# Optimization experiments

Measured on AMD Instinct MI355X. Metric: run time of the kernel, lower is better.

Reference implementation:

```python
import jax, jax.numpy as jnp
import numpy as np

H = 16      # n_heads
D = 1024    # d_model
DK = D // H # head dim


def setup_inputs() -> dict:
    key = jax.random.key(0)
    ks = jax.random.split(key, 11)
    B, S = 4, 2048
    std = 1.0 / np.sqrt(D)
    inp = {
        "query": jax.random.normal(ks[0], (B, S, D), jnp.float32),
        "key": jax.random.normal(ks[1], (B, S, D), jnp.float32),
        "value": jax.random.normal(ks[2], (B, S, D), jnp.float32),
        "Wq": jax.random.normal(ks[3], (D, D), jnp.float32) * std,
        "bq": jnp.zeros((D,), jnp.float32),
        "Wk": jax.random.normal(ks[4], (D, D), jnp.float32) * std,
        "bk": jnp.zeros((D,), jnp.float32),
        "Wv": jax.random.normal(ks[5], (D, D), jnp.float32) * std,
        "bv": jnp.zeros((D,), jnp.float32),
        "Wo": jax.random.normal(ks[6], (D, D), jnp.float32) * std,
        "bo": jnp.zeros((D,), jnp.float32),
    }
    return inp


def reference(query, key, value, Wq, bq, Wk, bk, Wv, bv, Wo, bo):
    B, S, _ = query.shape
    # QKV projections (nn.Linear), then split heads: [B, S, H, DK]
    q = (query @ Wq + bq).reshape(B, S, H, DK)
    k = (key @ Wk + bk).reshape(B, S, H, DK)
    v = (value @ Wv + bv).reshape(B, S, H, DK)
    # Memory-efficient attention computes exactly softmax(QK^T/sqrt(dk))V
    scale = 1.0 / np.sqrt(DK).astype(np.float32)
    scores = jnp.einsum("bqhd,bkhd->bhqk", q, k) * scale  # [B, H, S, S]
    attn = jax.nn.softmax(scores, axis=-1)
    x = jnp.einsum("bhqk,bkhd->bqhd", attn, v)            # [B, S, H, DK]
    x = x.reshape(B, S, H * DK)
    return x @ Wo + bo
```

## Files before the change

kernel.cpp:

```cpp
#include <hip/hip_runtime.h>
#include <hip/hip_bf16.h>

typedef short short8 __attribute__((ext_vector_type(8)));
typedef float f32x4 __attribute__((ext_vector_type(4)));
typedef float f32x16 __attribute__((ext_vector_type(16)));
typedef unsigned short u16;
typedef unsigned int u32;

#define HD 16
#define DMODEL 1024
#define DKH 64
#define SEQ 2048
#define QSCALE 0.18033688f

typedef const __attribute__((address_space(1))) void gvoid;
typedef __attribute__((address_space(3))) void lvoid;

__device__ inline u16 f2bf(float f) {
  unsigned int x = __builtin_bit_cast(unsigned int, f);
  unsigned int r = (x + 0x7fffu + ((x >> 16) & 1u)) >> 16;
  return (u16)r;
}

__device__ inline float fexp2(float x) {
#if __has_builtin(__builtin_amdgcn_exp2f)
  return __builtin_amdgcn_exp2f(x);
#else
  return __expf(x * 0.69314718f);
#endif
}

__device__ inline u32 cvtpk(float lo, float hi_) {
  u32 r;
  asm("v_cvt_pk_bf16_f32 %0, %1, %2" : "=v"(r) : "v"(lo), "v"(hi_));
  return r;
}

__device__ inline void pswap(u32& a, u32& b) {
  asm volatile("v_permlane32_swap_b32 %0, %1" : "+v"(a), "+v"(b));
}

__device__ inline f32x4 mfma16(short8 a, short8 b, f32x4 c) {
  return __builtin_amdgcn_mfma_f32_16x16x32_bf16(a, b, c, 0, 0, 0);
}
__device__ inline f32x16 mfma32(short8 a, short8 b, f32x16 c) {
  return __builtin_amdgcn_mfma_f32_32x32x16_bf16(a, b, c, 0, 0, 0);
}

__global__ __launch_bounds__(256) void prep_kernel(const float* __restrict__ q,
                                                   const float* __restrict__ k,
                                                   const float* __restrict__ v,
                                                   const float* __restrict__ W0,
                                                   const float* __restrict__ W1,
                                                   const float* __restrict__ W2,
                                                   const float* __restrict__ W3,
                                                   u16* __restrict__ Qf,
                                                   u16* __restrict__ Kf,
                                                   u16* __restrict__ Vf,
                                                   u16* __restrict__ WT) {
  const int z = blockIdx.z;
  if (z < 3) {
    const float* src = z == 0 ? q : z == 1 ? k : v;
    u16* dst = z == 0 ? Qf : z == 1 ? Kf : Vf;
    const int nthr = gridDim.x * 256;
    for (size_t i = blockIdx.x * 256 + threadIdx.x; i < (size_t)(SEQ * 4) * DMODEL / 8; i += nthr) {
      const float4 a0 = *(const float4*)(src + i * 8);
      const float4 a1 = *(const float4*)(src + i * 8 + 4);
      u32 tmp[4] = {cvtpk(a0.x, a0.y), cvtpk(a0.z, a0.w),
                    cvtpk(a1.x, a1.y), cvtpk(a1.z, a1.w)};
      *(uint4*)(dst + i * 8) = *(uint4*)tmp;
    }
  } else {
    __shared__ float tile[64][65];
    const int b = blockIdx.x;
    const int w = b >> 8;
    const int n0 = (b & 15) * 64, k0 = ((b >> 4) & 15) * 64;
    const float* W = w == 0 ? W0 : w == 1 ? W1 : w == 2 ? W2 : W3;
    u16* out = WT + (size_t)w * DMODEL * DMODEL;
    int tx = threadIdx.x & 63, ty = threadIdx.x >> 6;
    for (int i = 0; i < 16; i++) {
      int r = ty + i * 4;
      tile[r][tx] = W[(size_t)(k0 + r) * DMODEL + n0 + tx];
    }
    __syncthreads();
    for (int i = 0; i < 16; i++) {
      int r = ty + i * 4;
      out[(size_t)(n0 + r) * DMODEL + k0 + tx] = f2bf(tile[tx][r]);
    }
  }
}

__global__ __launch_bounds__(256, 2) void gemm_qkv(const u16* __restrict__ Qf,
                                                   const u16* __restrict__ Kf,
                                                   const u16* __restrict__ Vf,
                                                   const u16* __restrict__ WT,
                                                   const float* __restrict__ bq,
                                                   const float* __restrict__ bk,
                                                   const float* __restrict__ bv,
                                                   u16* __restrict__ Qb,
                                                   u16* __restrict__ Kb,
                                                   u16* __restrict__ Vtb) {
  __shared__ u16 As[2][128 * 64];
  __shared__ u16 Bs[2][128 * 64];
  const int b = blockIdx.x;
  const int xcd = b & 7, slot = b >> 3;
  const int nidx = slot & 7, pl = slot >> 3;
  const int pg = xcd * 24 + pl;
  const int z = pg >> 6, by = pg & 63;

  const u16* A = z == 0 ? Qf : z == 1 ? Kf : Vf;
  const u16* Bt = WT + (size_t)z * DMODEL * DMODEL;
  const float* bias = z == 0 ? bq : z == 1 ? bk : bv;
  u16* Cv = z == 0 ? Qb : z == 1 ? Kb : Vtb;
  const float scale = z == 0 ? QSCALE : 1.0f;
  const bool vtrans = (z == 2);

  const int m0 = by * 128, n0 = nidx * 128;
  const int tid = threadIdx.x;
  const int lane = tid & 63, wid = tid >> 6;
  const int g = lane >> 4, c = lane & 15;
  const int wr = (wid >> 1) * 64, wc = (wid & 1) * 64;

  const int trow = tid >> 3;
  const int tcolb = (tid & 7) << 4;
  const int swr = (c & 7) << 4;
  f32x4 acc[4][4] = {};

#define STAGE_AB(buf, kk0)                                                            \
  _Pragma("unroll") for (int p = 0; p < 4; ++p) {                                     \
    const int row = p * 32 + trow;                                                    \
    const int scol = tcolb ^ ((row & 7) << 4);                                        \
    __builtin_amdgcn_global_load_lds(                                                 \
        (gvoid*)((const char*)A + ((size_t)(m0 + row) * DMODEL + (kk0)) * 2 + scol),  \
        (lvoid*)((char*)&As[buf][0] + row * 128 + tcolb), 16, 0, 0);                  \
    __builtin_amdgcn_global_load_lds(                                                 \
        (gvoid*)((const char*)Bt + ((size_t)(n0 + row) * DMODEL + (kk0)) * 2 + scol), \
        (lvoid*)((char*)&Bs[buf][0] + row * 128 + tcolb), 16, 0, 0);                  \
  }

  STAGE_AB(0, 0);
  STAGE_AB(1, 64);
  __syncthreads();

  for (int t = 0; t < 16; ++t) {
    const int cur = t & 1;
    short8 af[4][2], bfr[4][2];
#pragma unroll
    for (int kk = 0; kk < 2; ++kk) {
#pragma unroll
      for (int mi = 0; mi < 4; ++mi)
        af[mi][kk] = *(const short8*)((const char*)&As[cur][0] + (wr + mi * 16 + c) * 128 + ((kk * 64 + g * 16) ^ swr));
#pragma unroll
      for (int ni = 0; ni < 4; ++ni)
        bfr[ni][kk] = *(const short8*)((const char*)&Bs[cur][0] + (wc + ni * 16 + c) * 128 + ((kk * 64 + g * 16) ^ swr));
    }
    __builtin_amdgcn_s_setprio(1);
#pragma unroll
    for (int kk = 0; kk < 2; ++kk)
#pragma unroll
      for (int mi = 0; mi < 4; ++mi)
#pragma unroll
        for (int ni = 0; ni < 4; ++ni)
          acc[mi][ni] = mfma16(af[mi][kk], bfr[ni][kk], acc[mi][ni]);
    __builtin_amdgcn_s_setprio(0);
    __syncthreads();
    if (t < 14) STAGE_AB(cur, (t + 2) * 64);
  }
#undef STAGE_AB

  for (int ni = 0; ni < 4; ++ni) {
    const int colg = n0 + wc + ni * 16 + c;
    const float bv_ = bias[colg];
    for (int mi = 0; mi < 4; ++mi) {
      const int rowb = m0 + wr + mi * 16 + g * 4;
      const int bb = rowb >> 11, s = rowb & 2047;
      const int h = colg >> 6, dk = colg & 63;
      if (!vtrans) {
        const size_t base = ((size_t)(bb * HD + h)) * SEQ;
        for (int j = 0; j < 4; ++j)
          Cv[(base + s + j) * DKH + dk] = f2bf((acc[mi][ni][j] + bv_) * scale);
      } else {
        const size_t base = ((size_t)(bb * HD + h) * DKH + dk) * SEQ + s;
        ushort4 u;
        u.x = f2bf(acc[mi][ni][0] + bv_);
        u.y = f2bf(acc[mi][ni][1] + bv_);
        u.z = f2bf(acc[mi][ni][2] + bv_);
        u.w = f2bf(acc[mi][ni][3] + bv_);
        *(ushort4*)(&Cv[base]) = u;
      }
    }
  }
}

__global__ __launch_bounds__(256, 2) void gemm_out(const u16* __restrict__ A,
                                                   const u16* __restrict__ Bt,
                                                   const float* __restrict__ bias,
                                                   float* __restrict__ C) {
  __shared__ u16 As[2][128 * 64];
  __shared__ u16 Bs[2][128 * 64];
  const int b = blockIdx.x;
  const int xcd = b & 7, slot = b >> 3;
  const int nidx = slot & 7, pl = slot >> 3;
  const int by = xcd * 8 + pl;

  const int m0 = by * 128, n0 = nidx * 128;
  const int tid = threadIdx.x;
  const int lane = tid & 63, wid = tid >> 6;
  const int g = lane >> 4, c = lane & 15;
  const int wr = (wid >> 1) * 64, wc = (wid & 1) * 64;

  const int trow = tid >> 3;
  const int tcolb = (tid & 7) << 4;
  const int swr = (c & 7) << 4;
  f32x4 acc[4][4] = {};

#define STAGE_AB(buf, kk0)                                                            \
  _Pragma("unroll") for (int p = 0; p < 4; ++p) {                                     \
    const int row = p * 32 + trow;                                                    \
    const int scol = tcolb ^ ((row & 7) << 4);                                        \
    __builtin_amdgcn_global_load_lds(                                                 \
        (gvoid*)((const char*)A + ((size_t)(m0 + row) * DMODEL + (kk0)) * 2 + scol),  \
        (lvoid*)((char*)&As[buf][0] + row * 128 + tcolb), 16, 0, 0);                  \
    __builtin_amdgcn_global_load_lds(                                                 \
        (gvoid*)((const char*)Bt + ((size_t)(n0 + row) * DMODEL + (kk0)) * 2 + scol), \
        (lvoid*)((char*)&Bs[buf][0] + row * 128 + tcolb), 16, 0, 0);                  \
  }

  STAGE_AB(0, 0);
  STAGE_AB(1, 64);
  __syncthreads();

  for (int t = 0; t < 16; ++t) {
    const int cur = t & 1;
    short8 af[4][2], bfr[4][2];
#pragma unroll
    for (int kk = 0; kk < 2; ++kk) {
#pragma unroll
      for (int mi = 0; mi < 4; ++mi)
        af[mi][kk] = *(const short8*)((const char*)&As[cur][0] + (wr + mi * 16 + c) * 128 + ((kk * 64 + g * 16) ^ swr));
#pragma unroll
      for (int ni = 0; ni < 4; ++ni)
        bfr[ni][kk] = *(const short8*)((const char*)&Bs[cur][0] + (wc + ni * 16 + c) * 128 + ((kk * 64 + g * 16) ^ swr));
    }
    __builtin_amdgcn_s_setprio(1);
#pragma unroll
    for (int kk = 0; kk < 2; ++kk)
#pragma unroll
      for (int mi = 0; mi < 4; ++mi)
#pragma unroll
        for (int ni = 0; ni < 4; ++ni)
          acc[mi][ni] = mfma16(af[mi][kk], bfr[ni][kk], acc[mi][ni]);
    __builtin_amdgcn_s_setprio(0);
    __syncthreads();
    if (t < 14) STAGE_AB(cur, (t + 2) * 64);
  }
#undef STAGE_AB

  for (int ni = 0; ni < 4; ++ni) {
    const int colg = n0 + wc + ni * 16 + c;
    const float bv = bias[colg];
    for (int mi = 0; mi < 4; ++mi) {
      const int rowb = m0 + wr + mi * 16 + g * 4;
      for (int j = 0; j < 4; ++j)
        C[(size_t)(rowb + j) * DMODEL + colg] = acc[mi][ni][j] + bv;
    }
  }
}

__global__ __launch_bounds__(256, 4) void attn_kernel(const u16* __restrict__ Q,
                                                      const u16* __restrict__ K,
                                                      const u16* __restrict__ Vt,
                                                      u16* __restrict__ X) {
  __shared__ char ldsmem[2][2][8192];
  const int tid = threadIdx.x;
  const int lane = tid & 63, wid = tid >> 6;
  const int c5 = lane & 31, hi = lane >> 5;

  const int blk = blockIdx.x;
  const int work = (blk & 7) * 128 + (blk >> 3);
  const int qt = work & 15, bh = work >> 4;

  const int q0 = qt * 128 + wid * 32;
  const u16* qb = Q + (size_t)bh * SEQ * DKH;
  const char* kbB = (const char*)(K + (size_t)bh * SEQ * DKH);
  const char* vbB = (const char*)(Vt + (size_t)bh * DKH * SEQ);

  short8 qf[4];
#pragma unroll
  for (int ks = 0; ks < 4; ++ks)
    qf[ks] = *(const short8*)(qb + (size_t)(q0 + c5) * DKH + ks * 16 + hi * 8);

  const int srow = tid >> 3;
  const int scolb = (tid & 7) << 4;
  const int scol = scolb ^ ((srow & 7) << 4);

  const int fswz = (c5 & 7) << 4;
  int cofs[4];
#pragma unroll
  for (int ks = 0; ks < 4; ++ks) cofs[ks] = ((ks * 32 + hi * 16) ^ fswz);

  f32x16 oacc[2] = {};
  float lrun = 0.f;

#pragma unroll
  for (int r32 = 0; r32 < 64; r32 += 32) {
    __builtin_amdgcn_global_load_lds(
        (gvoid*)(kbB + (size_t)(r32 + srow) * 128 + scol),
        (lvoid*)(&ldsmem[0][0][(r32 + srow) * 128 + scolb]), 16, 0, 0);
    __builtin_amdgcn_global_load_lds(
        (gvoid*)(vbB + (size_t)(r32 + srow) * (SEQ * 2) + scol),
        (lvoid*)(&ldsmem[0][1][(r32 + srow) * 128 + scolb]), 16, 0, 0);
  }
  __syncthreads();

#pragma unroll 2
  for (int t = 0; t < 32; ++t) {
    const int buf = t & 1;
    if (t < 31) {
      const size_t kv1 = (size_t)(t + 1) * 64;
#pragma unroll
      for (int r32 = 0; r32 < 64; r32 += 32) {
        __builtin_amdgcn_global_load_lds(
            (gvoid*)(kbB + (kv1 + r32 + srow) * 128 + scol),
            (lvoid*)(&ldsmem[buf ^ 1][0][(r32 + srow) * 128 + scolb]), 16, 0, 0);
        __builtin_amdgcn_global_load_lds(
            (gvoid*)(vbB + (size_t)(r32 + srow) * (SEQ * 2) + kv1 * 2 + scol),
            (lvoid*)(&ldsmem[buf ^ 1][1][(r32 + srow) * 128 + scolb]), 16, 0, 0);
      }
    }

    const char* bK = &ldsmem[buf][0][0];
    const char* bV = &ldsmem[buf][1][0];

    f32x16 sacc[2] = {};
#pragma unroll
    for (int kt = 0; kt < 2; ++kt) {
      short8 kf[4];
#pragma unroll
      for (int ks = 0; ks < 4; ++ks)
        kf[ks] = *(const short8*)(bK + (kt * 32 + c5) * 128 + cofs[ks]);
#pragma unroll
      for (int ks = 0; ks < 4; ++ks)
        sacc[kt] = mfma32(kf[ks], qf[ks], sacc[kt]);
    }

    float rs = 0.f;
    u32 W[2][8];
#pragma unroll
    for (int kt = 0; kt < 2; ++kt)
#pragma unroll
      for (int j = 0; j < 8; ++j) {
        float p0 = fexp2(sacc[kt][2 * j]);
        float p1 = fexp2(sacc[kt][2 * j + 1]);
        rs += p0 + p1;
        W[kt][j] = cvtpk(p0, p1);
      }
    rs += __shfl_xor(rs, 32, 64);
    lrun += rs;

    short8 pa[4];
#pragma unroll
    for (int ks = 0; ks < 4; ++ks) {
      const int kt = ks >> 1, l4 = (ks & 1) * 4;
      u32 a0 = W[kt][l4 + 0], b0 = W[kt][l4 + 2];
      u32 a1 = W[kt][l4 + 1], b1 = W[kt][l4 + 3];
      pswap(a0, b0);
      pswap(a1, b1);
      u32 tmp[4] = {a0, a1, b0, b1};
      pa[ks] = *(const short8*)tmp;
    }

    short8 vf[2][4];
#pragma unroll
    for (int dkt = 0; dkt < 2; ++dkt)
#pragma unroll
      for (int ks = 0; ks < 4; ++ks)
        vf[dkt][ks] = *(const short8*)(bV + (dkt * 32 + c5) * 128 + cofs[ks]);
#pragma unroll
    for (int ks = 0; ks < 4; ++ks)
#pragma unroll
      for (int dkt = 0; dkt < 2; ++dkt)
        oacc[dkt] = mfma32(pa[ks], vf[dkt][ks], oacc[dkt]);

    __syncthreads();
  }

  const int b = bh >> 4, h = bh & 15;
  const float inv = 1.0f / lrun;
#pragma unroll
  for (int r = 0; r < 16; ++r) {
    const int qrow = (r & 3) + 8 * (r >> 2) + 4 * hi;
    const float linv = __shfl(inv, qrow, 64);
    const size_t rowbase = ((size_t)(b * SEQ) + q0 + qrow) * DMODEL + h * DKH;
#pragma unroll
    for (int dkt = 0; dkt < 2; ++dkt)
      X[rowbase + dkt * 32 + c5] = f2bf(oacc[dkt][r] * linv);
  }
}

extern "C" void kernel_launch(void* const* d_in, const int* in_sizes, int n_in,
                              void* d_out, int out_size, void* d_ws, size_t ws_size,
                              hipStream_t stream) {
  (void)in_sizes; (void)n_in; (void)out_size; (void)ws_size;
  const float* query = (const float*)d_in[0];
  const float* key   = (const float*)d_in[1];
  const float* value = (const float*)d_in[2];
  const float* Wq = (const float*)d_in[3];
  const float* bq = (const float*)d_in[4];
  const float* Wk = (const float*)d_in[5];
  const float* bk = (const float*)d_in[6];
  const float* Wv = (const float*)d_in[7];
  const float* bv = (const float*)d_in[8];
  const float* Wo = (const float*)d_in[9];
  const float* bo = (const float*)d_in[10];
  float* out = (float*)d_out;

  char* ws = (char*)d_ws;
  const size_t MB = 1024 * 1024;
  u16* WT  = (u16*)ws;
  u16* Qf  = (u16*)(ws + 8 * MB);
  u16* Kf  = (u16*)(ws + 24 * MB);
  u16* Vf  = (u16*)(ws + 40 * MB);
  u16* Qb  = (u16*)(ws + 56 * MB);
  u16* Kb  = (u16*)(ws + 72 * MB);
  u16* Vtb = (u16*)(ws + 88 * MB);
  u16* Xb  = (u16*)(ws + 8 * MB);

  prep_kernel<<<dim3(1024, 1, 4), 256, 0, stream>>>(query, key, value, Wq, Wk, Wv, Wo,
                                                    Qf, Kf, Vf, WT);
  gemm_qkv<<<dim3(1536), 256, 0, stream>>>(Qf, Kf, Vf, WT, bq, bk, bv, Qb, Kb, Vtb);
  attn_kernel<<<dim3(1024), 256, 0, stream>>>(Qb, Kb, Vtb, Xb);
  gemm_out<<<dim3(512), 256, 0, stream>>>(Xb, WT + 3 * 1048576, bo, out);
}
```

Baseline: 189.3 us.

## Software-pipeline QK^T one tile ahead with triple-buffered V in attention

Restructures the attention loop so the QK^T MFMAs for tile t+1 are issued while the softmax exp and PV MFMAs for tile t run. K moves to a double buffer and V to a triple buffer, with prefetch two tiles ahead. The row-sum accumulation is split into four partial sums to shorten the dependency chain. The goal is more overlap between MFMA, exp/VALU and LDS loads, paid for with extra registers (two score accumulators live at once) and more LDS per block, which may lower occupancy.

After: 523.2 us. 176% more time.

```diff
diff --git a/kernel.cpp b/kernel.cpp
--- a/kernel.cpp
+++ b/kernel.cpp
@@ -271,7 +271,8 @@
                                                       const u16* __restrict__ K,
                                                       const u16* __restrict__ Vt,
                                                       u16* __restrict__ X) {
-  __shared__ char ldsmem[2][2][8192];
+  __shared__ char Kls[2][8192];
+  __shared__ char Vls[3][8192];
   const int tid = threadIdx.x;
   const int lane = tid & 63, wid = tid >> 6;
   const int c5 = lane & 31, hi = lane >> 5;
@@ -302,88 +303,85 @@
   f32x16 oacc[2] = {};
   float lrun = 0.f;
 
-#pragma unroll
-  for (int r32 = 0; r32 < 64; r32 += 32) {
-    __builtin_amdgcn_global_load_lds(
-        (gvoid*)(kbB + (size_t)(r32 + srow) * 128 + scol),
-        (lvoid*)(&ldsmem[0][0][(r32 + srow) * 128 + scolb]), 16, 0, 0);
-    __builtin_amdgcn_global_load_lds(
-        (gvoid*)(vbB + (size_t)(r32 + srow) * (SEQ * 2) + scol),
-        (lvoid*)(&ldsmem[0][1][(r32 + srow) * 128 + scolb]), 16, 0, 0);
-  }
+#define STAGE_K(t, dst)                                                         \
+  _Pragma("unroll") for (int r32 = 0; r32 < 64; r32 += 32)                      \
+      __builtin_amdgcn_global_load_lds(                                         \
+          (gvoid*)(kbB + ((size_t)(t) * 64 + r32 + srow) * 128 + scol),         \
+          (lvoid*)((dst) + (r32 + srow) * 128 + scolb), 16, 0, 0);
+#define STAGE_V(t, dst)                                                         \
+  _Pragma("unroll") for (int r32 = 0; r32 < 64; r32 += 32)                      \
+      __builtin_amdgcn_global_load_lds(                                         \
+          (gvoid*)(vbB + (size_t)(r32 + srow) * (SEQ * 2) + (size_t)(t) * 128 + scol), \
+          (lvoid*)((dst) + (r32 + srow) * 128 + scolb), 16, 0, 0);
+#define QKT(bufK, S)                                                            \
+  _Pragma("unroll") for (int kt = 0; kt < 2; ++kt) {                            \
+    short8 kf[4];                                                               \
+    _Pragma("unroll") for (int ks = 0; ks < 4; ++ks)                            \
+        kf[ks] = *(const short8*)((bufK) + (kt * 32 + c5) * 128 + cofs[ks]);    \
+    S[kt] = (f32x16){};                                                         \
+    _Pragma("unroll") for (int ks = 0; ks < 4; ++ks)                            \
+        S[kt] = mfma32(kf[ks], qf[ks], S[kt]);                                  \
+  }
+
+  STAGE_K(0, Kls[0]); STAGE_V(0, Vls[0]);
+  STAGE_K(1, Kls[1]); STAGE_V(1, Vls[1]);
   __syncthreads();
 
-#pragma unroll 2
-  for (int t = 0; t < 32; ++t) {
-    const int buf = t & 1;
-    if (t < 31) {
-      const size_t kv1 = (size_t)(t + 1) * 64;
-#pragma unroll
-      for (int r32 = 0; r32 < 64; r32 += 32) {
-        __builtin_amdgcn_global_load_lds(
-            (gvoid*)(kbB + (kv1 + r32 + srow) * 128 + scol),
-            (lvoid*)(&ldsmem[buf ^ 1][0][(r32 + srow) * 128 + scolb]), 16, 0, 0);
-        __builtin_amdgcn_global_load_lds(
-            (gvoid*)(vbB + (size_t)(r32 + srow) * (SEQ * 2) + kv1 * 2 + scol),
-            (lvoid*)(&ldsmem[buf ^ 1][1][(r32 + srow) * 128 + scolb]), 16, 0, 0);
-      }
-    }
-
-    const char* bK = &ldsmem[buf][0][0];
-    const char* bV = &ldsmem[buf][1][0];
-
-    f32x16 sacc[2] = {};
-#pragma unroll
-    for (int kt = 0; kt < 2; ++kt) {
-      short8 kf[4];
-#pragma unroll
-      for (int ks = 0; ks < 4; ++ks)
-        kf[ks] = *(const short8*)(bK + (kt * 32 + c5) * 128 + cofs[ks]);
-#pragma unroll
-      for (int ks = 0; ks < 4; ++ks)
-        sacc[kt] = mfma32(kf[ks], qf[ks], sacc[kt]);
-    }
-
-    float rs = 0.f;
-    u32 W[2][8];
-#pragma unroll
-    for (int kt = 0; kt < 2; ++kt)
-#pragma unroll
-      for (int j = 0; j < 8; ++j) {
-        float p0 = fexp2(sacc[kt][2 * j]);
-        float p1 = fexp2(sacc[kt][2 * j + 1]);
-        rs += p0 + p1;
-        W[kt][j] = cvtpk(p0, p1);
-      }
-    rs += __shfl_xor(rs, 32, 64);
-    lrun += rs;
-
-    short8 pa[4];
-#pragma unroll
-    for (int ks = 0; ks < 4; ++ks) {
-      const int kt = ks >> 1, l4 = (ks & 1) * 4;
-      u32 a0 = W[kt][l4 + 0], b0 = W[kt][l4 + 2];
-      u32 a1 = W[kt][l4 + 1], b1 = W[kt][l4 + 3];
-      pswap(a0, b0);
-      pswap(a1, b1);
-      u32 tmp[4] = {a0, a1, b0, b1};
-      pa[ks] = *(const short8*)tmp;
-    }
-
-    short8 vf[2][4];
-#pragma unroll
-    for (int dkt = 0; dkt < 2; ++dkt)
-#pragma unroll
-      for (int ks = 0; ks < 4; ++ks)
-        vf[dkt][ks] = *(const short8*)(bV + (dkt * 32 + c5) * 128 + cofs[ks]);
-#pragma unroll
-    for (int ks = 0; ks < 4; ++ks)
-#pragma unroll
-      for (int dkt = 0; dkt < 2; ++dkt)
-        oacc[dkt] = mfma32(pa[ks], vf[dkt][ks], oacc[dkt]);
-
-    __syncthreads();
-  }
+  f32x16 sA[2], sB[2];
+  QKT(Kls[0], sA);
+  __syncthreads();
+
+#define BODY(t, CUR, NXT, DO_STAGE, DO_QK)                                      \
+  {                                                                             \
+    if (DO_STAGE) {                                                             \
+      STAGE_K((t) + 2, Kls[(t) & 1]);                                           \
+      STAGE_V((t) + 2, Vls[((t) + 2) % 3]);                                     \
+    }                                                                           \
+    if (DO_QK) { QKT(Kls[((t) + 1) & 1], NXT); }                                \
+                          \
+    float rsx[4] = {0.f, 0.f, 0.f, 0.f};                                        \
+    u32 W[2][8];                                                                \
+    _Pragma("unroll") for (int kt = 0; kt < 2; ++kt)                            \
+    _Pragma("unroll") for (int j = 0; j < 8; ++j) {                             \
+      float p0 = fexp2(CUR[kt][2 * j]);                                         \
+      float p1 = fexp2(CUR[kt][2 * j + 1]);                                     \
+      rsx[(kt * 8 + j) & 3] += p0 + p1;                                         \
+      W[kt][j] = cvtpk(p0, p1);                                                 \
+    }                                                                           \
+    float rs = (rsx[0] + rsx[1]) + (rsx[2] + rsx[3]);                           \
+    rs += __shfl_xor(rs, 32, 64);                                               \
+    lrun += rs;                                                                 \
+    short8 pa[4];                                                               \
+    _Pragma("unroll") for (int ks = 0; ks < 4; ++ks) {                          \
+      const int kt = ks >> 1, l4 = (ks & 1) * 4;                                \
+      u32 a0 = W[kt][l4 + 0], b0 = W[kt][l4 + 2];                               \
+      u32 a1 = W[kt][l4 + 1], b1 = W[kt][l4 + 3];                               \
+      pswap(a0, b0);                                                            \
+      pswap(a1, b1);                                                            \
+      u32 tmp[4] = {a0, a1, b0, b1};                                            \
+      pa[ks] = *(const short8*)tmp;                                             \
+    }                                                                           \
+    const char* bV = Vls[(t) % 3];                                              \
+    _Pragma("unroll") for (int ks = 0; ks < 4; ++ks)                            \
+    _Pragma("unroll") for (int dkt = 0; dkt < 2; ++dkt) {                       \
+      short8 vf = *(const short8*)(bV + (dkt * 32 + c5) * 128 + cofs[ks]);      \
+      oacc[dkt] = mfma32(pa[ks], vf, oacc[dkt]);                                \
+    }                                                                           \
+    __syncthreads();                                                            \
+  }
+
+  for (int tt = 0; tt < 15; ++tt) {
+    const int t0 = tt * 2;
+    BODY(t0, sA, sB, 1, 1);
+    BODY(t0 + 1, sB, sA, 1, 1);
+  }
+  BODY(30, sA, sB, 0, 1);
+  BODY(31, sB, sA, 0, 0);
+
+#undef BODY
+#undef QKT
+#undef STAGE_K
+#undef STAGE_V
 
   const int b = bh >> 4, h = bh & 15;
   const float inv = 1.0f / lrun;
```

## Software-pipeline attention loop: compute next QK^T alongside current PV with deeper prefetch

Applied to the files above, without the earlier changes.

Restructures the attention loop so the QK^T scores for tile t+1 are computed while the softmax and PV of tile t are in flight. K and V are now staged two tiles ahead, with K double-buffered and V triple-buffered, and the pointers rotate each iteration. s_setprio is raised around the MFMA sections so waves overlap exp work with matrix work. The intent is to hide the exp and LDS latency behind MFMA; the cost is more LDS (40KB per block) and more live registers, which may reduce occupancy at launch_bounds(256,4).

Result: no change. 190.0 us (+0.4%).

```diff
diff --git a/kernel.cpp b/kernel.cpp
--- a/kernel.cpp
+++ b/kernel.cpp
@@ -271,7 +271,8 @@
                                                       const u16* __restrict__ K,
                                                       const u16* __restrict__ Vt,
                                                       u16* __restrict__ X) {
-  __shared__ char ldsmem[2][2][8192];
+  __shared__ char Kls[2][8192];
+  __shared__ char Vls[3][8192];
   const int tid = threadIdx.x;
   const int lane = tid & 63, wid = tid >> 6;
   const int c5 = lane & 31, hi = lane >> 5;
@@ -300,48 +301,45 @@
   for (int ks = 0; ks < 4; ++ks) cofs[ks] = ((ks * 32 + hi * 16) ^ fswz);
 
   f32x16 oacc[2] = {};
+  f32x16 sacc[2];
   float lrun = 0.f;
 
-#pragma unroll
-  for (int r32 = 0; r32 < 64; r32 += 32) {
-    __builtin_amdgcn_global_load_lds(
-        (gvoid*)(kbB + (size_t)(r32 + srow) * 128 + scol),
-        (lvoid*)(&ldsmem[0][0][(r32 + srow) * 128 + scolb]), 16, 0, 0);
-    __builtin_amdgcn_global_load_lds(
-        (gvoid*)(vbB + (size_t)(r32 + srow) * (SEQ * 2) + scol),
-        (lvoid*)(&ldsmem[0][1][(r32 + srow) * 128 + scolb]), 16, 0, 0);
-  }
+#define STAGE_K(t, dst)                                                         \
+  _Pragma("unroll") for (int r32 = 0; r32 < 64; r32 += 32)                      \
+      __builtin_amdgcn_global_load_lds(                                         \
+          (gvoid*)(kbB + ((size_t)(t) * 64 + r32 + srow) * 128 + scol),         \
+          (lvoid*)((dst) + (r32 + srow) * 128 + scolb), 16, 0, 0);
+#define STAGE_V(t, dst)                                                         \
+  _Pragma("unroll") for (int r32 = 0; r32 < 64; r32 += 32)                      \
+      __builtin_amdgcn_global_load_lds(                                         \
+          (gvoid*)(vbB + (size_t)(r32 + srow) * (SEQ * 2) + (size_t)(t) * 128 + scol), \
+          (lvoid*)((dst) + (r32 + srow) * 128 + scolb), 16, 0, 0);
+#define QKT(bufK)                                                               \
+  _Pragma("unroll") for (int kt = 0; kt < 2; ++kt) {                            \
+    short8 kf[4];                                                               \
+    _Pragma("unroll") for (int ks = 0; ks < 4; ++ks)                            \
+        kf[ks] = *(const short8*)((bufK) + (kt * 32 + c5) * 128 + cofs[ks]);    \
+    sacc[kt] = (f32x16){};                                                      \
+    _Pragma("unroll") for (int ks = 0; ks < 4; ++ks)                            \
+        sacc[kt] = mfma32(kf[ks], qf[ks], sacc[kt]);                            \
+  }
+
+  STAGE_K(0, Kls[0]); STAGE_V(0, Vls[0]);
+  STAGE_K(1, Kls[1]); STAGE_V(1, Vls[1]);
   __syncthreads();
-
-#pragma unroll 2
+  QKT(Kls[0]);
+  __syncthreads();
+
+  char* pk_nxt = Kls[1];
+  char* pk_stg = Kls[0];
+  char* pv_cur = Vls[0];
+  char* pv_nxt = Vls[1];
+  char* pv_stg = Vls[2];
+
   for (int t = 0; t < 32; ++t) {
-    const int buf = t & 1;
-    if (t < 31) {
-      const size_t kv1 = (size_t)(t + 1) * 64;
-#pragma unroll
-      for (int r32 = 0; r32 < 64; r32 += 32) {
-        __builtin_amdgcn_global_load_lds(
-            (gvoid*)(kbB + (kv1 + r32 + srow) * 128 + scol),
-            (lvoid*)(&ldsmem[buf ^ 1][0][(r32 + srow) * 128 + scolb]), 16, 0, 0);
-        __builtin_amdgcn_global_load_lds(
-            (gvoid*)(vbB + (size_t)(r32 + srow) * (SEQ * 2) + kv1 * 2 + scol),
-            (lvoid*)(&ldsmem[buf ^ 1][1][(r32 + srow) * 128 + scolb]), 16, 0, 0);
-      }
-    }
-
-    const char* bK = &ldsmem[buf][0][0];
-    const char* bV = &ldsmem[buf][1][0];
-
-    f32x16 sacc[2] = {};
-#pragma unroll
-    for (int kt = 0; kt < 2; ++kt) {
-      short8 kf[4];
-#pragma unroll
-      for (int ks = 0; ks < 4; ++ks)
-        kf[ks] = *(const short8*)(bK + (kt * 32 + c5) * 128 + cofs[ks]);
-#pragma unroll
-      for (int ks = 0; ks < 4; ++ks)
-        sacc[kt] = mfma32(kf[ks], qf[ks], sacc[kt]);
+    if (t < 30) {
+      STAGE_K(t + 2, pk_stg);
+      STAGE_V(t + 2, pv_stg);
     }
 
     float rs = 0.f;
@@ -370,20 +368,31 @@
       pa[ks] = *(const short8*)tmp;
     }
 
-    short8 vf[2][4];
-#pragma unroll
-    for (int dkt = 0; dkt < 2; ++dkt)
-#pragma unroll
-      for (int ks = 0; ks < 4; ++ks)
-        vf[dkt][ks] = *(const short8*)(bV + (dkt * 32 + c5) * 128 + cofs[ks]);
+    if (t < 31) {
+      __builtin_amdgcn_s_setprio(1);
+      QKT(pk_nxt);
+      __builtin_amdgcn_s_setprio(0);
+    }
+
+    __builtin_amdgcn_s_setprio(1);
 #pragma unroll
     for (int ks = 0; ks < 4; ++ks)
 #pragma unroll
-      for (int dkt = 0; dkt < 2; ++dkt)
-        oacc[dkt] = mfma32(pa[ks], vf[dkt][ks], oacc[dkt]);
+      for (int dkt = 0; dkt < 2; ++dkt) {
+        short8 vf = *(const short8*)(pv_cur + (dkt * 32 + c5) * 128 + cofs[ks]);
+        oacc[dkt] = mfma32(pa[ks], vf, oacc[dkt]);
+      }
+    __builtin_amdgcn_s_setprio(0);
 
     __syncthreads();
-  }
+
+    char* tk = pk_nxt; pk_nxt = pk_stg; pk_stg = tk;
+    char* tv = pv_cur; pv_cur = pv_nxt; pv_nxt = pv_stg; pv_stg = tv;
+  }
+
+#undef QKT
+#undef STAGE_K
+#undef STAGE_V
 
   const int b = bh >> 4, h = bh & 15;
   const float inv = 1.0f / lrun;
```
